# Performance work log

Measured on AMD Instinct MI355X. Metric: run time of the kernel, lower is better.

Reference implementation:

```python
import jax, jax.numpy as jnp
import numpy as np

# Mamba2 dims (match init_kwargs)
DM = 1024          # d_model
EXPAND = 2
D_INNER = EXPAND * DM            # 2048 (== d_ssm)
HEADDIM = 64
NHEADS = D_INNER // HEADDIM      # 32
DSTATE = 128
NGROUPS = 1
DCONV = 4
CONV_DIM = D_INNER + 2 * NGROUPS * DSTATE        # 2304
D_IN_PROJ = 2 * D_INNER + 2 * NGROUPS * DSTATE + NHEADS  # 4384
BATCH, SEQ = 4, 1024
EPS = 1e-5


def setup_inputs() -> dict:
    key = jax.random.key(0)
    ks = jax.random.split(key, 8)
    x = jax.random.normal(ks[0], (BATCH, SEQ, DM), dtype=jnp.float32)
    in_proj_w = jax.random.normal(ks[1], (D_IN_PROJ, DM), dtype=jnp.float32) * 0.02
    conv_w = jax.random.normal(ks[2], (CONV_DIM, 1, DCONV), dtype=jnp.float32) * 0.2
    conv_b = jnp.zeros((CONV_DIM,), dtype=jnp.float32)
    # dt_bias = inv_softplus(dt) with dt ~ logU[dt_min, dt_max]
    dt = jnp.exp(jax.random.uniform(ks[3], (NHEADS,)) * (np.log(0.1) - np.log(0.001)) + np.log(0.001))
    dt_bias = dt + jnp.log(-jnp.expm1(-dt))
    # A ~ U[1, 16], A_log = log(A)
    A_log = jnp.log(jax.random.uniform(ks[4], (NHEADS,), minval=1.0, maxval=16.0))
    D = jnp.ones((NHEADS,), dtype=jnp.float32)
    norm_w = jnp.ones((D_INNER,), dtype=jnp.float32)
    out_proj_w = jax.random.normal(ks[5], (DM, D_INNER), dtype=jnp.float32) * 0.02
    return {"x": x, "in_proj_w": in_proj_w, "conv_w": conv_w, "conv_b": conv_b,
            "dt_bias": dt_bias, "A_log": A_log, "D": D, "norm_w": norm_w,
            "out_proj_w": out_proj_w}


def _mamba2_forward(x, in_proj_w, conv_w, conv_b, dt_bias, A_log, D, norm_w, out_proj_w):
    B, L, _ = x.shape
    zxbcdt = jnp.einsum('bld,ed->ble', x, in_proj_w)  # (B,L,D_IN_PROJ)
    z = zxbcdt[..., :D_INNER]
    xBC = zxbcdt[..., D_INNER:D_INNER + CONV_DIM]
    dt_raw = zxbcdt[..., D_INNER + CONV_DIM:]         # (B,L,NHEADS)

    # causal depthwise conv1d + silu
    xt = jnp.transpose(xBC, (0, 2, 1))                # (B, CONV_DIM, L)
    conv = jax.lax.conv_general_dilated(
        xt, conv_w, window_strides=(1,), padding=[(DCONV - 1, 0)],
        dimension_numbers=('NCH', 'OIH', 'NCH'), feature_group_count=CONV_DIM)
    conv = conv + conv_b[None, :, None]
    xBC = jnp.transpose(jax.nn.silu(conv), (0, 2, 1))  # (B,L,CONV_DIM)

    x_ssm = xBC[..., :D_INNER].reshape(B, L, NHEADS, HEADDIM)
    Bm = xBC[..., D_INNER:D_INNER + NGROUPS * DSTATE].reshape(B, L, NGROUPS, DSTATE)
    Cm = xBC[..., D_INNER + NGROUPS * DSTATE:].reshape(B, L, NGROUPS, DSTATE)

    dt = jax.nn.softplus(dt_raw + dt_bias)            # (B,L,H)
    A = -jnp.exp(A_log)                               # (H,)
    dA = jnp.exp(dt * A)                              # (B,L,H)
    dtx = dt[..., None] * x_ssm                       # (B,L,H,P)

    rep = NHEADS // NGROUPS
    Bh = jnp.repeat(Bm, rep, axis=2)                  # (B,L,H,N)
    Ch = jnp.repeat(Cm, rep, axis=2)

    def step(h, inp):
        dA_t, dtx_t, B_t, C_t = inp
        h = dA_t[:, :, None, None] * h + dtx_t[..., None] * B_t[:, :, None, :]
        y = jnp.einsum('bhpn,bhn->bhp', h, C_t)
        return h, y

    h0 = jnp.zeros((B, NHEADS, HEADDIM, DSTATE), dtype=x.dtype)
    xs = (jnp.transpose(dA, (1, 0, 2)),
          jnp.transpose(dtx, (1, 0, 2, 3)),
          jnp.transpose(Bh, (1, 0, 2, 3)),
          jnp.transpose(Ch, (1, 0, 2, 3)))
    _, ys = jax.lax.scan(step, h0, xs)                # (L,B,H,P)
    y = jnp.transpose(ys, (1, 0, 2, 3)) + D[None, None, :, None] * x_ssm
    y = y.reshape(B, L, D_INNER)

    # gated RMSNorm (norm_before_gate=False): normalize(y * silu(z)) * w
    yz = y * jax.nn.silu(z)
    yz = yz * jax.lax.rsqrt(jnp.mean(yz * yz, axis=-1, keepdims=True) + EPS) * norm_w

    return jnp.einsum('bld,ed->ble', yz, out_proj_w)  # (B,L,DM)


def reference(x, in_proj_w, conv_w, conv_b, dt_bias, A_log, D, norm_w, out_proj_w):
    return _mamba2_forward(x, in_proj_w, conv_w, conv_b, dt_bias, A_log, D, norm_w, out_proj_w)
```

## Files before the change

kernel.cpp:

```cpp
#include <hip/hip_runtime.h>
#include <hip/hip_bf16.h>

#define DM        1024
#define D_INNER   2048
#define NHEADS    32
#define HEADDIM   64
#define DSTATE    128
#define DCONV     4
#define CONV_DIM  (D_INNER + 2*DSTATE)
#define D_IN_PROJ (2*D_INNER + 2*DSTATE + NHEADS)
#define NPAD_IN   4480
#define BATCH     4
#define SEQ       1024
#define NROWS     (BATCH*SEQ)
#define EPSF      1e-5f
#define CHUNK     128
#define NCHUNK    (SEQ/CHUNK)
#define BH        (BATCH*NHEADS)

#define OFF_ZX   ((size_t)0)
#define OFF_XBC  ((size_t)(NROWS)*D_IN_PROJ)
#define OFF_DT   (OFF_XBC + (size_t)NROWS*CONV_DIM)
#define OFF_DA   (OFF_DT  + (size_t)NROWS*NHEADS)
#define OFF_Y    (OFF_DA  + (size_t)NROWS*NHEADS)
#define FLOAT_END (OFF_Y + (size_t)NROWS*D_INNER)
#define SOFF_XB   ((size_t)0)
#define SOFF_W1B  (SOFF_XB  + (size_t)NROWS*DM)
#define SOFF_W2B  (SOFF_W1B + (size_t)NPAD_IN*DM)
#define SOFF_YZB  (SOFF_W2B + (size_t)DM*D_INNER)
#define HD_SHORTS ((size_t)NCHUNK*BH*HEADDIM*DSTATE)

typedef float  vf4   __attribute__((ext_vector_type(4)));
typedef short  s16x8 __attribute__((ext_vector_type(8)));
typedef short  s16x4 __attribute__((ext_vector_type(4)));
typedef __bf16 bf16x8 __attribute__((ext_vector_type(8)));

__device__ __forceinline__ float sigmoidf_(float x) { return 1.f / (1.f + expf(-x)); }

__device__ __forceinline__ short f2bf(float f) {
    unsigned u = __builtin_bit_cast(unsigned, f);
    u += 0x7fffu + ((u >> 16) & 1u);
    return (short)(u >> 16);
}
__device__ __forceinline__ float bf2f(short s) {
    unsigned u = ((unsigned)(unsigned short)s) << 16;
    return __builtin_bit_cast(float, u);
}
__device__ __forceinline__ bf16x8 as_bf(s16x8 v) { return __builtin_bit_cast(bf16x8, v); }
#define MFMA(a,b,c) __builtin_amdgcn_mfma_f32_16x16x32_bf16(as_bf(a), as_bf(b), (c), 0, 0, 0)

__device__ __forceinline__ void gload16(const short* g, short* l) {
    __builtin_amdgcn_global_load_lds(
        (const __attribute__((address_space(1))) unsigned int*)g,
        (__attribute__((address_space(3))) unsigned int*)l, 16, 0, 0);
}

__device__ __forceinline__ int swz_idx(int r, int kc) {
    return r * 128 + (((kc) ^ (r & 7)) << 3);
}
__device__ __forceinline__ void stage_tile(const float* __restrict__ g, int gstride,
                                           short* __restrict__ lds, int rows, int tid) {
    for (int s = tid; s < rows * 16; s += 512) {
        int r = s >> 4, c = s & 15;
        const float* p = g + (size_t)r * gstride + c * 8;
        float4 v0 = *(const float4*)p, v1 = *(const float4*)(p + 4);
        s16x8 o;
        o[0]=f2bf(v0.x); o[1]=f2bf(v0.y); o[2]=f2bf(v0.z); o[3]=f2bf(v0.w);
        o[4]=f2bf(v1.x); o[5]=f2bf(v1.y); o[6]=f2bf(v1.z); o[7]=f2bf(v1.w);
        *(s16x8*)&lds[swz_idx(r, c)] = o;
    }
}

__global__ __launch_bounds__(256) void cvt_bf16(const float* __restrict__ src,
                                                short* __restrict__ dst,
                                                int n_src, int n_dst) {
    int i = (blockIdx.x * 256 + threadIdx.x) * 4;
    if (i >= n_dst) return;
    s16x4 o;
    if (i + 3 < n_src) {
        float4 v = *(const float4*)(src + i);
        o[0] = f2bf(v.x); o[1] = f2bf(v.y); o[2] = f2bf(v.z); o[3] = f2bf(v.w);
    } else {
        #pragma unroll
        for (int j = 0; j < 4; ++j) o[j] = (i + j < n_src) ? f2bf(src[i + j]) : (short)0;
    }
    *(s16x4*)(dst + i) = o;
}

__global__ __launch_bounds__(256) void gemm_mfma(const short* __restrict__ A,
                                                 const short* __restrict__ B,
                                                 float* __restrict__ C,
                                                 int M, int K, int Nout) {
    __shared__ short smem[16384];
    const int tid = threadIdx.x;
    const int bm = blockIdx.y * 128, bn = blockIdx.x * 128;
    const int lane = tid & 63, lr = lane & 15, lg = lane >> 4;
    const int w = tid >> 6, wm = w >> 1, wn = w & 1;

    const short* ga[4]; const short* gb[4];
    short* la[4]; short* lb[4];
    #pragma unroll
    for (int t = 0; t < 4; ++t) {
        int s = t * 256 + tid;
        int r = s >> 3;
        int c = (s & 7) ^ (r & 7);
        ga[t] = A + (size_t)(bm + r) * K + c * 8;
        gb[t] = B + (size_t)(bn + r) * K + c * 8;
        la[t] = &smem[s * 8];
        lb[t] = &smem[8192 + s * 8];
    }

    vf4 acc[4][4] = {};

    for (int k0 = 0; k0 < K; k0 += 64) {
        __syncthreads();
        #pragma unroll
        for (int t = 0; t < 4; ++t) gload16(ga[t] + k0, la[t]);
        #pragma unroll
        for (int t = 0; t < 4; ++t) gload16(gb[t] + k0, lb[t]);
        __syncthreads();
        #pragma unroll
        for (int kk = 0; kk < 2; ++kk) {
            const int co = ((kk * 4 + lg) ^ (lr & 7)) * 8;
            s16x8 av[4], bv[4];
            #pragma unroll
            for (int f = 0; f < 4; ++f) {
                av[f] = *(const s16x8*)&smem[(wm * 64 + f * 16 + lr) * 64 + co];
                bv[f] = *(const s16x8*)&smem[8192 + (wn * 64 + f * 16 + lr) * 64 + co];
            }
            #pragma unroll
            for (int i = 0; i < 4; ++i)
                #pragma unroll
                for (int j = 0; j < 4; ++j)
                    acc[i][j] = MFMA(av[i], bv[j], acc[i][j]);
        }
    }

    #pragma unroll
    for (int i = 0; i < 4; ++i) {
        int row = bm + wm * 64 + i * 16 + lg * 4;
        #pragma unroll
        for (int j = 0; j < 4; ++j) {
            int col = bn + wn * 64 + j * 16 + lr;
            if (col < Nout) {
                float* cp = C + (size_t)row * Nout + col;
                #pragma unroll
                for (int q = 0; q < 4; ++q) cp[(size_t)q * Nout] = acc[i][j][q];
            }
        }
    }
}

__global__ __launch_bounds__(256) void conv_silu(const float* __restrict__ zx,
                                                 const float* __restrict__ cw,
                                                 const float* __restrict__ cb,
                                                 float* __restrict__ xBC) {
    int idx = blockIdx.x * 256 + threadIdx.x;
    if (idx >= NROWS * CONV_DIM) return;
    int c  = idx % CONV_DIM;
    int bl = idx / CONV_DIM;
    int b  = bl / SEQ;
    int l  = bl % SEQ;

    float w0 = cw[c*4+0], w1 = cw[c*4+1], w2 = cw[c*4+2], w3 = cw[c*4+3];
    const float* base = zx + (size_t)b * SEQ * D_IN_PROJ + D_INNER + c;

    float acc = cb[c];
    if (l >= 3) acc = fmaf(base[(size_t)(l-3) * D_IN_PROJ], w0, acc);
    if (l >= 2) acc = fmaf(base[(size_t)(l-2) * D_IN_PROJ], w1, acc);
    if (l >= 1) acc = fmaf(base[(size_t)(l-1) * D_IN_PROJ], w2, acc);
    acc = fmaf(base[(size_t)l * D_IN_PROJ], w3, acc);

    xBC[idx] = acc * sigmoidf_(acc);
}

__global__ __launch_bounds__(256) void dt_da(const float* __restrict__ zx,
                                             const float* __restrict__ dt_bias,
                                             float* __restrict__ dt) {
    int idx = blockIdx.x * 256 + threadIdx.x;
    if (idx >= NROWS * NHEADS) return;
    int h  = idx & (NHEADS - 1);
    int bl = idx >> 5;
    float u = zx[(size_t)bl * D_IN_PROJ + D_INNER + CONV_DIM + h] + dt_bias[h];
    float d = (u > 20.f) ? u : log1pf(expf(u));
    dt[idx] = d;
}

#define L_CT 0
#define L_BT 16384
#define L_BW 32768
#define L_XT 49152
__global__ __launch_bounds__(512) void ssm_mfma_a(const float* __restrict__ xBC,
                                                  const float* __restrict__ dt,
                                                  const float* __restrict__ A_log,
                                                  const float* __restrict__ Dp,
                                                  float* __restrict__ y,
                                                  short* __restrict__ hd16,
                                                  float* __restrict__ datot) {
    __shared__ short sm[57344];
    __shared__ float dtl[128], lcs[128];
    int blk = blockIdx.x;
    int h = blk & 31, k = (blk >> 5) & (NCHUNK - 1), b = blk >> 8;
    int tid = threadIdx.x, w = tid >> 6, lane = tid & 63, lr = lane & 15, lg = lane >> 4;
    int bl0 = b * SEQ + k * CHUNK;
    const float* xrow = xBC + (size_t)bl0 * CONV_DIM;

    if (tid < 128) dtl[tid] = dt[(size_t)(bl0 + tid) * NHEADS + h];
    __syncthreads();

    stage_tile(xrow + D_INNER + DSTATE, CONV_DIM, sm + L_CT, 128, tid);
    stage_tile(xrow + D_INNER,          CONV_DIM, sm + L_BT, 128, tid);
    for (int s = tid; s < 64 * 16; s += 512) {
        int p = s >> 4, jc = s & 15;
        s16x8 o;
        #pragma unroll
        for (int jj = 0; jj < 8; ++jj) {
            int j = jc * 8 + jj;
            o[jj] = f2bf(dtl[j] * xrow[(size_t)j * CONV_DIM + h * HEADDIM + p]);
        }
        *(s16x8*)&sm[L_XT + swz_idx(p, jc)] = o;
    }
    __syncthreads();

    float Ah = -__expf(A_log[h]);
    if (w == 0) {
        float a = dtl[lane], bb = dtl[64 + lane];
        #pragma unroll
        for (int d = 1; d < 64; d <<= 1) { float v = __shfl_up(a, d);  if (lane >= d) a  += v; }
        #pragma unroll
        for (int d = 1; d < 64; d <<= 1) { float v = __shfl_up(bb, d); if (lane >= d) bb += v; }
        bb += __shfl(a, 63);
        lcs[lane]      = Ah * a;
        lcs[64 + lane] = Ah * bb;
        if (lane == 63) datot[k * BH + b * NHEADS + h] = __expf(Ah * bb);
    }
    __syncthreads();
    float lcLast = lcs[127];

    for (int s = tid; s < 128 * 16; s += 512) {
        int n = s >> 4, jc = s & 15;
        s16x8 o;
        #pragma unroll
        for (int jj = 0; jj < 8; ++jj) {
            int j = jc * 8 + jj;
            float bv = bf2f(sm[L_BT + swz_idx(j, n >> 3) + (n & 7)]);
            o[jj] = f2bf(bv * __expf(lcLast - lcs[j]));
        }
        *(s16x8*)&sm[L_BW + swz_idx(n, jc)] = o;
    }
    vf4 g[2][4] = {};
    const int rb = (w & 3) * 32, cb = (w >> 2) * 64;
    #pragma unroll
    for (int ks = 0; ks < 4; ++ks) {
        int kc = ks * 4 + lg;
        s16x8 av[2], bv[4];
        #pragma unroll
        for (int i = 0; i < 2; ++i) { int r = rb + i * 16 + lr; av[i] = *(const s16x8*)&sm[L_CT + swz_idx(r, kc)]; }
        #pragma unroll
        for (int jf = 0; jf < 4; ++jf) { int r = cb + jf * 16 + lr; bv[jf] = *(const s16x8*)&sm[L_BT + swz_idx(r, kc)]; }
        #pragma unroll
        for (int i = 0; i < 2; ++i)
            #pragma unroll
            for (int jf = 0; jf < 4; ++jf)
                g[i][jf] = MFMA(av[i], bv[jf], g[i][jf]);
    }
    __syncthreads();

    #pragma unroll
    for (int i = 0; i < 2; ++i)
        #pragma unroll
        for (int jf = 0; jf < 4; ++jf)
            #pragma unroll
            for (int q = 0; q < 4; ++q) {
                int t = rb + i * 16 + lg * 4 + q;
                int j = cb + jf * 16 + lr;
                float v = (j <= t) ? g[i][jf][q] * __expf(lcs[t] - lcs[j]) : 0.f;
                sm[L_BT + swz_idx(t, j >> 3) + (j & 7)] = f2bf(v);
            }
    __syncthreads();

    vf4 yi[2][2] = {};
    vf4 hdl[4] = {};
    const int prb = (w >> 2) * 32;
    const int hrb = (w & 3) * 16;
    const int hcb = (w >> 2) * 64;
    #pragma unroll
    for (int ks = 0; ks < 4; ++ks) {
        int kc = ks * 4 + lg;
        s16x8 am[2], bx[2], ax, bw[4];
        #pragma unroll
        for (int i = 0; i < 2; ++i)  { int r = rb + i * 16 + lr;  am[i]  = *(const s16x8*)&sm[L_BT + swz_idx(r, kc)]; }
        #pragma unroll
        for (int jf = 0; jf < 2; ++jf){ int r = prb + jf * 16 + lr; bx[jf] = *(const s16x8*)&sm[L_XT + swz_idx(r, kc)]; }
        { int r = hrb + lr; ax = *(const s16x8*)&sm[L_XT + swz_idx(r, kc)]; }
        #pragma unroll
        for (int jf = 0; jf < 4; ++jf){ int r = hcb + jf * 16 + lr; bw[jf] = *(const s16x8*)&sm[L_BW + swz_idx(r, kc)]; }
        #pragma unroll
        for (int i = 0; i < 2; ++i)
            #pragma unroll
            for (int jf = 0; jf < 2; ++jf)
                yi[i][jf] = MFMA(am[i], bx[jf], yi[i][jf]);
        #pragma unroll
        for (int jf = 0; jf < 4; ++jf)
            hdl[jf] = MFMA(ax, bw[jf], hdl[jf]);
    }

    float Dh = Dp[h];
    #pragma unroll
    for (int i = 0; i < 2; ++i)
        #pragma unroll
        for (int jf = 0; jf < 2; ++jf)
            #pragma unroll
            for (int q = 0; q < 4; ++q) {
                int t = rb + i * 16 + lg * 4 + q;
                int p = prb + jf * 16 + lr;
                float xv = xrow[(size_t)t * CONV_DIM + h * HEADDIM + p];
                y[(size_t)(bl0 + t) * D_INNER + h * HEADDIM + p] = yi[i][jf][q] + Dh * xv;
            }
    size_t hb = ((size_t)k * BH + b * NHEADS + h) * (HEADDIM * DSTATE);
    #pragma unroll
    for (int jf = 0; jf < 4; ++jf)
        #pragma unroll
        for (int q = 0; q < 4; ++q) {
            int p = hrb + lg * 4 + q;
            int n = hcb + jf * 16 + lr;
            hd16[hb + p * DSTATE + n] = f2bf(hdl[jf][q]);
        }
}

__global__ __launch_bounds__(512) void ssm_state_b(short* __restrict__ hd16,
                                                   const float* __restrict__ datot) {
    int bh = blockIdx.x;
    int base = threadIdx.x * 16;
    float hs[16];
    #pragma unroll
    for (int i = 0; i < 16; ++i) hs[i] = 0.f;
    #pragma unroll
    for (int k = 0; k < NCHUNK; ++k) {
        size_t off = ((size_t)k * BH + bh) * (HEADDIM * DSTATE) + base;
        float da = datot[k * BH + bh];
        s16x8 d0 = *(const s16x8*)&hd16[off], d1 = *(const s16x8*)&hd16[off + 8];
        s16x8 o0, o1;
        #pragma unroll
        for (int i = 0; i < 8; ++i) { o0[i] = f2bf(hs[i]); o1[i] = f2bf(hs[8 + i]); }
        *(s16x8*)&hd16[off] = o0; *(s16x8*)&hd16[off + 8] = o1;
        #pragma unroll
        for (int i = 0; i < 8; ++i) {
            hs[i]     = fmaf(da, hs[i],     bf2f(d0[i]));
            hs[8 + i] = fmaf(da, hs[8 + i], bf2f(d1[i]));
        }
    }
}

__global__ __launch_bounds__(512) void ssm_mfma_c(const float* __restrict__ xBC,
                                                  const float* __restrict__ dt,
                                                  const float* __restrict__ A_log,
                                                  const short* __restrict__ hd16,
                                                  float* __restrict__ y) {
    int blk = blockIdx.x;
    int h = blk & 31, k = (blk >> 5) & (NCHUNK - 1), b = blk >> 8;
    if (k == 0) return;
    __shared__ short sm[16384];
    __shared__ float dtl[128], lcs[128];
    int tid = threadIdx.x, w = tid >> 6, lane = tid & 63, lr = lane & 15, lg = lane >> 4;
    int bl0 = b * SEQ + k * CHUNK;
    const float* xrow = xBC + (size_t)bl0 * CONV_DIM;

    if (tid < 128) dtl[tid] = dt[(size_t)(bl0 + tid) * NHEADS + h];
    __syncthreads();
    stage_tile(xrow + D_INNER + DSTATE, CONV_DIM, sm, 128, tid);
    float Ah = -__expf(A_log[h]);
    __syncthreads();
    if (w == 0) {
        float a = dtl[lane], bb = dtl[64 + lane];
        #pragma unroll
        for (int d = 1; d < 64; d <<= 1) { float v = __shfl_up(a, d);  if (lane >= d) a  += v; }
        #pragma unroll
        for (int d = 1; d < 64; d <<= 1) { float v = __shfl_up(bb, d); if (lane >= d) bb += v; }
        bb += __shfl(a, 63);
        lcs[lane]      = Ah * a;
        lcs[64 + lane] = Ah * bb;
    }
    __syncthreads();

    const short* hin = hd16 + ((size_t)k * BH + b * NHEADS + h) * (HEADDIM * DSTATE);
    vf4 yi[2][2] = {};
    const int rb = (w & 3) * 32, prb = (w >> 2) * 32;
    #pragma unroll
    for (int ks = 0; ks < 4; ++ks) {
        int kc = ks * 4 + lg;
        s16x8 av[2], bv[2];
        #pragma unroll
        for (int i = 0; i < 2; ++i)  { int r = rb + i * 16 + lr; av[i] = *(const s16x8*)&sm[swz_idx(r, kc)]; }
        #pragma unroll
        for (int jf = 0; jf < 2; ++jf){
            int p = prb + jf * 16 + lr;
            bv[jf] = *(const s16x8*)&hin[p * DSTATE + ks * 32 + lg * 8];
        }
        #pragma unroll
        for (int i = 0; i < 2; ++i)
            #pragma unroll
            for (int jf = 0; jf < 2; ++jf)
                yi[i][jf] = MFMA(av[i], bv[jf], yi[i][jf]);
    }
    #pragma unroll
    for (int i = 0; i < 2; ++i)
        #pragma unroll
        for (int jf = 0; jf < 2; ++jf)
            #pragma unroll
            for (int q = 0; q < 4; ++q) {
                int t = rb + i * 16 + lg * 4 + q;
                int p = prb + jf * 16 + lr;
                float* yp = y + (size_t)(bl0 + t) * D_INNER + h * HEADDIM + p;
                *yp = fmaf(__expf(lcs[t]), yi[i][jf][q], *yp);
            }
}

__global__ __launch_bounds__(256) void gate_rmsnorm(const float* __restrict__ y,
                                                    const float* __restrict__ zx,
                                                    const float* __restrict__ nw,
                                                    short* __restrict__ yzb) {
    int bl = blockIdx.x;
    const float* yr = y + (size_t)bl * D_INNER;
    const float* zr = zx + (size_t)bl * D_IN_PROJ;
    int e0 = threadIdx.x * 8;

    float4 y0 = *(const float4*)(yr + e0);
    float4 y1 = *(const float4*)(yr + e0 + 4);
    float4 z0 = *(const float4*)(zr + e0);
    float4 z1 = *(const float4*)(zr + e0 + 4);

    float v[8];
    float zz[8] = {z0.x, z0.y, z0.z, z0.w, z1.x, z1.y, z1.z, z1.w};
    float yy[8] = {y0.x, y0.y, y0.z, y0.w, y1.x, y1.y, y1.z, y1.w};
    float ss = 0.f;
    #pragma unroll
    for (int i = 0; i < 8; ++i) {
        v[i] = yy[i] * zz[i] * sigmoidf_(zz[i]);
        ss = fmaf(v[i], v[i], ss);
    }
    ss += __shfl_xor(ss, 1);  ss += __shfl_xor(ss, 2);  ss += __shfl_xor(ss, 4);
    ss += __shfl_xor(ss, 8);  ss += __shfl_xor(ss, 16); ss += __shfl_xor(ss, 32);
    __shared__ float red[4];
    int wave = threadIdx.x >> 6;
    if ((threadIdx.x & 63) == 0) red[wave] = ss;
    __syncthreads();
    ss = red[0] + red[1] + red[2] + red[3];

    float scale = rsqrtf(ss * (1.f / D_INNER) + EPSF);
    s16x8 o;
    #pragma unroll
    for (int i = 0; i < 8; ++i) o[i] = f2bf(v[i] * scale * nw[e0 + i]);
    *(s16x8*)(yzb + (size_t)bl * D_INNER + e0) = o;
}

extern "C" void kernel_launch(void* const* d_in, const int* in_sizes, int n_in,
                              void* d_out, int out_size, void* d_ws, size_t ws_size,
                              hipStream_t stream) {
    const float* x        = (const float*)d_in[0];
    const float* in_w     = (const float*)d_in[1];
    const float* conv_w   = (const float*)d_in[2];
    const float* conv_b   = (const float*)d_in[3];
    const float* dt_bias  = (const float*)d_in[4];
    const float* A_log    = (const float*)d_in[5];
    const float* Dp       = (const float*)d_in[6];
    const float* norm_w   = (const float*)d_in[7];
    const float* out_w    = (const float*)d_in[8];
    float* out            = (float*)d_out;

    float* ws   = (float*)d_ws;
    float* zx   = ws + OFF_ZX;
    float* xBC  = ws + OFF_XBC;
    float* dt   = ws + OFF_DT;
    float* y    = ws + OFF_Y;
    short* sb   = (short*)(ws + FLOAT_END);
    short* xb   = sb + SOFF_XB;
    short* w1b  = sb + SOFF_W1B;
    short* w2b  = sb + SOFF_W2B;
    short* yzb  = sb + SOFF_YZB;
    short* hd16  = xb;
    float* datot = (float*)(hd16 + HD_SHORTS);

    {
        int n = NROWS * DM;
        cvt_bf16<<<n / 4 / 256, 256, 0, stream>>>(x, xb, n, n);
        int ns = D_IN_PROJ * DM, nd = NPAD_IN * DM;
        cvt_bf16<<<nd / 4 / 256, 256, 0, stream>>>(in_w, w1b, ns, nd);
        int n2 = DM * D_INNER;
        cvt_bf16<<<n2 / 4 / 256, 256, 0, stream>>>(out_w, w2b, n2, n2);
    }
    {
        dim3 grid(NPAD_IN / 128, NROWS / 128);
        gemm_mfma<<<grid, 256, 0, stream>>>(xb, w1b, zx, NROWS, DM, D_IN_PROJ);
    }
    {
        int total = NROWS * CONV_DIM;
        conv_silu<<<(total + 255) / 256, 256, 0, stream>>>(zx, conv_w, conv_b, xBC);
    }
    {
        int total = NROWS * NHEADS;
        dt_da<<<(total + 255) / 256, 256, 0, stream>>>(zx, dt_bias, dt);
    }
    ssm_mfma_a<<<BATCH * NCHUNK * NHEADS, 512, 0, stream>>>(xBC, dt, A_log, Dp, y, hd16, datot);
    ssm_state_b<<<BH, 512, 0, stream>>>(hd16, datot);
    ssm_mfma_c<<<BATCH * NCHUNK * NHEADS, 512, 0, stream>>>(xBC, dt, A_log, hd16, y);
    gate_rmsnorm<<<NROWS, 256, 0, stream>>>(y, zx, norm_w, yzb);
    {
        dim3 grid(DM / 128, NROWS / 128);
        gemm_mfma<<<grid, 256, 0, stream>>>(yzb, w2b, out, NROWS, D_INNER, DM);
    }
}
```

Baseline: 364.3 us.

## Run chunk SSM kernel with 1024 threads and coalesced x staging

Doubles the block size of the intra-chunk SSM kernel to 1024 threads and splits the MFMA work so each wave holds fewer accumulator tiles. x is now loaded with coalesced float4 reads into a row-major LDS tile, then transposed and scaled by dt inside LDS instead of through strided global reads. The C·B^T MFMA is moved ahead of the cumulative-sum barrier so it overlaps with the scan, and one barrier is dropped. The risk is lower occupancy per CU with 1024-thread blocks and the LDS reuse of the C region for the transposed x.

```diff
diff --git a/kernel.cpp b/kernel.cpp
--- a/kernel.cpp
+++ b/kernel.cpp
@@ -58,9 +58,13 @@
 __device__ __forceinline__ int swz_idx(int r, int kc) {
     return r * 128 + (((kc) ^ (r & 7)) << 3);
 }
+__device__ __forceinline__ int swz64_idx(int r, int c) {
+    return r * 64 + (((c) ^ (r & 7)) << 3);
+}
 __device__ __forceinline__ void stage_tile(const float* __restrict__ g, int gstride,
-                                           short* __restrict__ lds, int rows, int tid) {
-    for (int s = tid; s < rows * 16; s += 512) {
+                                           short* __restrict__ lds, int rows,
+                                           int tid, int nthr) {
+    for (int s = tid; s < rows * 16; s += nthr) {
         int r = s >> 4, c = s & 15;
         const float* p = g + (size_t)r * gstride + c * 8;
         float4 v0 = *(const float4*)p, v1 = *(const float4*)(p + 4);
@@ -187,16 +191,17 @@
 }
 
 #define L_CT 0
+#define L_XT 0
 #define L_BT 16384
 #define L_BW 32768
-#define L_XT 49152
-__global__ __launch_bounds__(512) void ssm_mfma_a(const float* __restrict__ xBC,
-                                                  const float* __restrict__ dt,
-                                                  const float* __restrict__ A_log,
-                                                  const float* __restrict__ Dp,
-                                                  float* __restrict__ y,
-                                                  short* __restrict__ hd16,
-                                                  float* __restrict__ datot) {
+#define L_XN 49152
+__global__ __launch_bounds__(1024) void ssm_mfma_a(const float* __restrict__ xBC,
+                                                   const float* __restrict__ dt,
+                                                   const float* __restrict__ A_log,
+                                                   const float* __restrict__ Dp,
+                                                   float* __restrict__ y,
+                                                   short* __restrict__ hd16,
+                                                   float* __restrict__ datot) {
     __shared__ short sm[57344];
     __shared__ float dtl[128], lcs[128];
     int blk = blockIdx.x;
@@ -206,19 +211,17 @@
     const float* xrow = xBC + (size_t)bl0 * CONV_DIM;
 
     if (tid < 128) dtl[tid] = dt[(size_t)(bl0 + tid) * NHEADS + h];
-    __syncthreads();
-
-    stage_tile(xrow + D_INNER + DSTATE, CONV_DIM, sm + L_CT, 128, tid);
-    stage_tile(xrow + D_INNER,          CONV_DIM, sm + L_BT, 128, tid);
-    for (int s = tid; s < 64 * 16; s += 512) {
-        int p = s >> 4, jc = s & 15;
+
+    stage_tile(xrow + D_INNER + DSTATE, CONV_DIM, sm + L_CT, 128, tid, 1024);
+    stage_tile(xrow + D_INNER,          CONV_DIM, sm + L_BT, 128, tid, 1024);
+    {
+        int r = tid >> 3, c = tid & 7;
+        const float* p = xrow + (size_t)r * CONV_DIM + h * HEADDIM + c * 8;
+        float4 v0 = *(const float4*)p, v1 = *(const float4*)(p + 4);
         s16x8 o;
-        #pragma unroll
-        for (int jj = 0; jj < 8; ++jj) {
-            int j = jc * 8 + jj;
-            o[jj] = f2bf(dtl[j] * xrow[(size_t)j * CONV_DIM + h * HEADDIM + p]);
-        }
-        *(s16x8*)&sm[L_XT + swz_idx(p, jc)] = o;
+        o[0]=f2bf(v0.x); o[1]=f2bf(v0.y); o[2]=f2bf(v0.z); o[3]=f2bf(v0.w);
+        o[4]=f2bf(v1.x); o[5]=f2bf(v1.y); o[6]=f2bf(v1.z); o[7]=f2bf(v1.w);
+        *(s16x8*)&sm[L_XN + swz64_idx(r, c)] = o;
     }
     __syncthreads();
 
@@ -234,92 +237,89 @@
         lcs[64 + lane] = Ah * bb;
         if (lane == 63) datot[k * BH + b * NHEADS + h] = __expf(Ah * bb);
     }
-    __syncthreads();
+
+    vf4 g[4] = {};
+    const int rb = (w & 7) * 16, cb = (w >> 3) * 64;
+    #pragma unroll
+    for (int ks = 0; ks < 4; ++ks) {
+        int kc = ks * 4 + lg;
+        s16x8 av = *(const s16x8*)&sm[L_CT + swz_idx(rb + lr, kc)];
+        #pragma unroll
+        for (int jf = 0; jf < 4; ++jf) {
+            s16x8 bv = *(const s16x8*)&sm[L_BT + swz_idx(cb + jf * 16 + lr, kc)];
+            g[jf] = MFMA(av, bv, g[jf]);
+        }
+    }
+    __syncthreads();
+
     float lcLast = lcs[127];
 
-    for (int s = tid; s < 128 * 16; s += 512) {
-        int n = s >> 4, jc = s & 15;
+    {
+        int p = tid & 63, c2 = tid >> 6;
         s16x8 o;
         #pragma unroll
         for (int jj = 0; jj < 8; ++jj) {
-            int j = jc * 8 + jj;
+            int j = c2 * 8 + jj;
+            float xv = bf2f(sm[L_XN + swz64_idx(j, p >> 3) + (p & 7)]);
+            o[jj] = f2bf(dtl[j] * xv);
+        }
+        *(s16x8*)&sm[L_XT + swz_idx(p, c2)] = o;
+    }
+    for (int s = tid; s < 2048; s += 1024) {
+        int n = s & 127, c = s >> 7;
+        s16x8 o;
+        #pragma unroll
+        for (int jj = 0; jj < 8; ++jj) {
+            int j = c * 8 + jj;
             float bv = bf2f(sm[L_BT + swz_idx(j, n >> 3) + (n & 7)]);
             o[jj] = f2bf(bv * __expf(lcLast - lcs[j]));
         }
-        *(s16x8*)&sm[L_BW + swz_idx(n, jc)] = o;
-    }
-    vf4 g[2][4] = {};
-    const int rb = (w & 3) * 32, cb = (w >> 2) * 64;
+        *(s16x8*)&sm[L_BW + swz_idx(n, c)] = o;
+    }
+    __syncthreads();
+
+    #pragma unroll
+    for (int jf = 0; jf < 4; ++jf)
+        #pragma unroll
+        for (int q = 0; q < 4; ++q) {
+            int t = rb + lg * 4 + q;
+            int j = cb + jf * 16 + lr;
+            float v = (j <= t) ? g[jf][q] * __expf(lcs[t] - lcs[j]) : 0.f;
+            sm[L_BT + swz_idx(t, j >> 3) + (j & 7)] = f2bf(v);
+        }
+    __syncthreads();
+
+    vf4 yi[2] = {};
+    vf4 hdl[2] = {};
+    const int rb2 = (w & 7) * 16, prb = (w >> 3) * 32;
+    const int hrb = (w & 3) * 16, hcb = (w >> 2) * 32;
     #pragma unroll
     for (int ks = 0; ks < 4; ++ks) {
         int kc = ks * 4 + lg;
-        s16x8 av[2], bv[4];
-        #pragma unroll
-        for (int i = 0; i < 2; ++i) { int r = rb + i * 16 + lr; av[i] = *(const s16x8*)&sm[L_CT + swz_idx(r, kc)]; }
-        #pragma unroll
-        for (int jf = 0; jf < 4; ++jf) { int r = cb + jf * 16 + lr; bv[jf] = *(const s16x8*)&sm[L_BT + swz_idx(r, kc)]; }
-        #pragma unroll
-        for (int i = 0; i < 2; ++i)
-            #pragma unroll
-            for (int jf = 0; jf < 4; ++jf)
-                g[i][jf] = MFMA(av[i], bv[jf], g[i][jf]);
-    }
-    __syncthreads();
-
-    #pragma unroll
-    for (int i = 0; i < 2; ++i)
-        #pragma unroll
-        for (int jf = 0; jf < 4; ++jf)
-            #pragma unroll
-            for (int q = 0; q < 4; ++q) {
-                int t = rb + i * 16 + lg * 4 + q;
-                int j = cb + jf * 16 + lr;
-                float v = (j <= t) ? g[i][jf][q] * __expf(lcs[t] - lcs[j]) : 0.f;
-                sm[L_BT + swz_idx(t, j >> 3) + (j & 7)] = f2bf(v);
-            }
-    __syncthreads();
-
-    vf4 yi[2][2] = {};
-    vf4 hdl[4] = {};
-    const int prb = (w >> 2) * 32;
-    const int hrb = (w & 3) * 16;
-    const int hcb = (w >> 2) * 64;
-    #pragma unroll
-    for (int ks = 0; ks < 4; ++ks) {
-        int kc = ks * 4 + lg;
-        s16x8 am[2], bx[2], ax, bw[4];
-        #pragma unroll
-        for (int i = 0; i < 2; ++i)  { int r = rb + i * 16 + lr;  am[i]  = *(const s16x8*)&sm[L_BT + swz_idx(r, kc)]; }
-        #pragma unroll
-        for (int jf = 0; jf < 2; ++jf){ int r = prb + jf * 16 + lr; bx[jf] = *(const s16x8*)&sm[L_XT + swz_idx(r, kc)]; }
-        { int r = hrb + lr; ax = *(const s16x8*)&sm[L_XT + swz_idx(r, kc)]; }
-        #pragma unroll
-        for (int jf = 0; jf < 4; ++jf){ int r = hcb + jf * 16 + lr; bw[jf] = *(const s16x8*)&sm[L_BW + swz_idx(r, kc)]; }
-        #pragma unroll
-        for (int i = 0; i < 2; ++i)
-            #pragma unroll
-            for (int jf = 0; jf < 2; ++jf)
-                yi[i][jf] = MFMA(am[i], bx[jf], yi[i][jf]);
-        #pragma unroll
-        for (int jf = 0; jf < 4; ++jf)
-            hdl[jf] = MFMA(ax, bw[jf], hdl[jf]);
+        s16x8 am = *(const s16x8*)&sm[L_BT + swz_idx(rb2 + lr, kc)];
+        s16x8 ax = *(const s16x8*)&sm[L_XT + swz_idx(hrb + lr, kc)];
+        #pragma unroll
+        for (int jf = 0; jf < 2; ++jf) {
+            s16x8 bx = *(const s16x8*)&sm[L_XT + swz_idx(prb + jf * 16 + lr, kc)];
+            s16x8 bw = *(const s16x8*)&sm[L_BW + swz_idx(hcb + jf * 16 + lr, kc)];
+            yi[jf]  = MFMA(am, bx, yi[jf]);
+            hdl[jf] = MFMA(ax, bw, hdl[jf]);
+        }
     }
 
     float Dh = Dp[h];
     #pragma unroll
-    for (int i = 0; i < 2; ++i)
-        #pragma unroll
-        for (int jf = 0; jf < 2; ++jf)
-            #pragma unroll
-            for (int q = 0; q < 4; ++q) {
-                int t = rb + i * 16 + lg * 4 + q;
-                int p = prb + jf * 16 + lr;
-                float xv = xrow[(size_t)t * CONV_DIM + h * HEADDIM + p];
-                y[(size_t)(bl0 + t) * D_INNER + h * HEADDIM + p] = yi[i][jf][q] + Dh * xv;
-            }
+    for (int jf = 0; jf < 2; ++jf)
+        #pragma unroll
+        for (int q = 0; q < 4; ++q) {
+            int t = rb2 + lg * 4 + q;
+            int p = prb + jf * 16 + lr;
+            float xv = xrow[(size_t)t * CONV_DIM + h * HEADDIM + p];
+            y[(size_t)(bl0 + t) * D_INNER + h * HEADDIM + p] = yi[jf][q] + Dh * xv;
+        }
     size_t hb = ((size_t)k * BH + b * NHEADS + h) * (HEADDIM * DSTATE);
     #pragma unroll
-    for (int jf = 0; jf < 4; ++jf)
+    for (int jf = 0; jf < 2; ++jf)
         #pragma unroll
         for (int q = 0; q < 4; ++q) {
             int p = hrb + lg * 4 + q;
@@ -368,7 +368,7 @@
 
     if (tid < 128) dtl[tid] = dt[(size_t)(bl0 + tid) * NHEADS + h];
     __syncthreads();
-    stage_tile(xrow + D_INNER + DSTATE, CONV_DIM, sm, 128, tid);
+    stage_tile(xrow + D_INNER + DSTATE, CONV_DIM, sm, 128, tid, 512);
     float Ah = -__expf(A_log[h]);
     __syncthreads();
     if (w == 0) {
@@ -501,7 +501,7 @@
         int total = NROWS * NHEADS;
         dt_da<<<(total + 255) / 256, 256, 0, stream>>>(zx, dt_bias, dt);
     }
-    ssm_mfma_a<<<BATCH * NCHUNK * NHEADS, 512, 0, stream>>>(xBC, dt, A_log, Dp, y, hd16, datot);
+    ssm_mfma_a<<<BATCH * NCHUNK * NHEADS, 1024, 0, stream>>>(xBC, dt, A_log, Dp, y, hd16, datot);
     ssm_state_b<<<BH, 512, 0, stream>>>(hd16, datot);
     ssm_mfma_c<<<BATCH * NCHUNK * NHEADS, 512, 0, stream>>>(xBC, dt, A_log, hd16, y);
     gate_rmsnorm<<<NROWS, 256, 0, stream>>>(y, zx, norm_w, yzb);
```

Result: faster. 337.7 us (-7.3%).
